# Optimization experiments

Measured on AMD Instinct MI355X. Metric: run time of the kernel, lower is better.

## Reference

```python
import jax, jax.numpy as jnp
import numpy as np

DIM = 1024
HEADS = 16
HEAD_DIM = DIM // HEADS
NUM_FILTERS = 4
NUM_TAPS = 101
RES = 512

def setup_inputs() -> dict:
    key = jax.random.key(0)
    ks = jax.random.split(key, 5)
    B, S = 2, 2048
    x = jax.random.normal(ks[0], (B, S, DIM), dtype=jnp.float32)
    Wqkv = jax.random.normal(ks[1], (3 * DIM, DIM), dtype=jnp.float32) * (DIM ** -0.5)
    Wout = jax.random.normal(ks[2], (DIM, DIM), dtype=jnp.float32) * (DIM ** -0.5)
    Wpos = jax.random.normal(ks[3], (HEADS, NUM_FILTERS), dtype=jnp.float32) * 0.5
    coeffs = jax.random.normal(ks[4], (NUM_FILTERS, NUM_TAPS), dtype=jnp.float32) * 0.05
    return {"x": x, "Wqkv": Wqkv, "Wout": Wout, "Wpos": Wpos, "coeffs": coeffs}

def _fir_fft(c, sig):
    # c: (T,), sig: (R,) -> causal FFT convolution, first R samples
    R = sig.shape[0]
    L = R + c.shape[0] - 1
    out = jnp.fft.ifft(jnp.fft.fft(sig, n=L) * jnp.fft.fft(c, n=L)).real
    return out[:R]

def reference(x, Wqkv, Wout, Wpos, coeffs):
    B, S, D = x.shape
    scale = HEAD_DIM ** -0.5

    # filtered prototype table: (R, F)
    proto = jnp.linspace(0.0, 1.0, RES).astype(x.dtype)
    table = jax.vmap(_fir_fft, in_axes=(0, None))(coeffs, proto).T  # (R, F)

    # relative-distance index matrix (S, S), constants derived from static shape
    r = jnp.arange(S)
    rel = jnp.abs(r[None, :] - r[:, None]).astype(jnp.float32) / max(S - 1, 1)
    idx = jnp.clip(jnp.round(rel * (RES - 1)).astype(jnp.int32), 0, RES - 1)

    pos_feat = table[idx]                                   # (S, S, F)
    pos_bias = jnp.einsum('ijf,hf->hij', pos_feat, Wpos)    # (H, S, S)

    qkv = jnp.einsum('bsd,ed->bse', x, Wqkv)                # (B, S, 3D)
    q, k, v = jnp.split(qkv, 3, axis=-1)
    q = q.reshape(B, S, HEADS, HEAD_DIM)
    k = k.reshape(B, S, HEADS, HEAD_DIM)
    v = v.reshape(B, S, HEADS, HEAD_DIM)

    logits = jnp.einsum('bihd,bjhd->bhij', q, k) * scale + pos_bias[None]
    attn = jax.nn.softmax(logits, axis=-1)
    out = jnp.einsum('bhij,bjhd->bihd', attn, v).reshape(B, S, D)
    return jnp.einsum('bsd,ed->bse', out, Wout)
```

## Files before the change

kernel.cpp:

```cpp
#include <hip/hip_runtime.h>
#include <hip/hip_bf16.h>
#include <cstddef>

#define SEQ     2048
#define BATCH   2
#define DIMSZ   1024
#define HEADS   16
#define HDIM    64
#define E3      3072
#define RESN    512
#define NTAPS   101
#define NFILT   4
#define MROWS   (BATCH * SEQ)
#define LOG2E   1.44269504088896340736f

typedef __attribute__((ext_vector_type(8))) short bf16x8;
typedef __attribute__((ext_vector_type(4))) float f32x4;

__device__ __forceinline__ unsigned short f2bf(float f) {
  unsigned u = __float_as_uint(f);
  u += 0x7fffu + ((u >> 16) & 1u);
  return (unsigned short)(u >> 16);
}
__device__ __forceinline__ float bf2f(unsigned short h) {
  return __uint_as_float(((unsigned)h) << 16);
}
__device__ __forceinline__ void split2(float f, unsigned short& h, unsigned short& l) {
  h = f2bf(f);
  l = f2bf(f - bf2f(h));
}
__device__ __forceinline__ unsigned pkbf(float a, float b) {
  __hip_bfloat162 t = __float22bfloat162_rn(float2{a, b});
  union { __hip_bfloat162 h; unsigned u; } cv; cv.h = t;
  return cv.u;
}
__device__ __forceinline__ void async16(void* lds, const void* g) {
  __builtin_amdgcn_global_load_lds(
      (const __attribute__((address_space(1))) unsigned int*)g,
      (__attribute__((address_space(3))) unsigned int*)lds, 16, 0, 0);
}

__global__ __launch_bounds__(256) void cvt_bf16_kern(
    const float* __restrict__ src, unsigned short* __restrict__ dst, int n)
{
  const int i = (blockIdx.x * 256 + threadIdx.x) * 8;
  if (i >= n) return;
  const float4 a = *(const float4*)(src + i);
  const float4 b = *(const float4*)(src + i + 4);
  ushort4 p = {f2bf(a.x), f2bf(a.y), f2bf(a.z), f2bf(a.w)};
  ushort4 q = {f2bf(b.x), f2bf(b.y), f2bf(b.z), f2bf(b.w)};
  *(ushort4*)(dst + i)     = p;
  *(ushort4*)(dst + i + 4) = q;
}

__global__ __launch_bounds__(256) void split_pair_kern(
    const float* __restrict__ src, unsigned short* __restrict__ hi,
    unsigned short* __restrict__ lo, int n)
{
  const int i = (blockIdx.x * 256 + threadIdx.x) * 4;
  if (i >= n) return;
  const float4 a = *(const float4*)(src + i);
  ushort4 h, l;
  split2(a.x, h.x, l.x); split2(a.y, h.y, l.y);
  split2(a.z, h.z, l.z); split2(a.w, h.w, l.w);
  *(ushort4*)(hi + i) = h;
  *(ushort4*)(lo + i) = l;
}

__global__ __launch_bounds__(256) void pbias_kernel(
    const float* __restrict__ coeffs, const float* __restrict__ Wpos,
    float* __restrict__ pbias2)
{
  __shared__ float table[RESN][NFILT];
  const int h = blockIdx.x;
  const int tid = threadIdx.x;
  for (int rf = tid; rf < RESN * NFILT; rf += 256) {
    const int r = rf >> 2, f = rf & 3;
    const int tmax = r < (NTAPS - 1) ? r : (NTAPS - 1);
    float s = 0.f;
    for (int t = 0; t <= tmax; ++t)
      s += coeffs[f * NTAPS + t] * ((float)(r - t) * (1.0f / (float)(RESN - 1)));
    table[r][f] = s;
  }
  __syncthreads();
  float wp[NFILT];
#pragma unroll
  for (int f = 0; f < NFILT; ++f) wp[f] = Wpos[h * NFILT + f];
  for (int d = tid; d < SEQ; d += 256) {
    const float rel = (float)d / (float)(SEQ - 1);
    int idx = (int)rintf(rel * (float)(RESN - 1));
    idx = idx < 0 ? 0 : (idx > RESN - 1 ? RESN - 1 : idx);
    float s = 0.f;
#pragma unroll
    for (int f = 0; f < NFILT; ++f) s += table[idx][f] * wp[f];
    pbias2[h * SEQ + d] = s * LOG2E;
  }
}

__global__ __launch_bounds__(256) void gemm_bf16(
    const unsigned short* __restrict__ A, const unsigned short* __restrict__ B,
    unsigned short* __restrict__ C, int M, int N, int K)
{
  __shared__ unsigned short As[128][32];
  __shared__ unsigned short Bs[128][32];
  const int tid = threadIdx.x;
  const int lane = tid & 63;
  const int w = tid >> 6, wm = w >> 1, wn = w & 1;
  const int c = lane & 15, G = lane >> 4;
  const int m0 = blockIdx.y * 128, n0 = blockIdx.x * 128;

  const int srow = lane >> 2;
  const int scol = (lane & 3) << 3;

  f32x4 acc[4][4];
#pragma unroll
  for (int mf = 0; mf < 4; ++mf)
#pragma unroll
    for (int nf = 0; nf < 4; ++nf) acc[mf][nf] = (f32x4){0.f, 0.f, 0.f, 0.f};

  for (int k0 = 0; k0 < K; k0 += 32) {
    __syncthreads();
#pragma unroll
    for (int r = 0; r < 2; ++r) {
      const int chunk = r * 4 + w;
      const int row = (chunk << 4) + srow;
      async16(&As[chunk << 4][0], A + (size_t)(m0 + row) * K + k0 + scol);
      async16(&Bs[chunk << 4][0], B + (size_t)(n0 + row) * K + k0 + scol);
    }
    __syncthreads();

    bf16x8 fa[4], fb[4];
#pragma unroll
    for (int mf = 0; mf < 4; ++mf)
      fa[mf] = *(const bf16x8*)&As[wm * 64 + 16 * mf + c][8 * G];
#pragma unroll
    for (int nf = 0; nf < 4; ++nf)
      fb[nf] = *(const bf16x8*)&Bs[wn * 64 + 16 * nf + c][8 * G];
#pragma unroll
    for (int nf = 0; nf < 4; ++nf)
#pragma unroll
      for (int mf = 0; mf < 4; ++mf)
        acc[mf][nf] = __builtin_amdgcn_mfma_f32_16x16x32_bf16(fa[mf], fb[nf], acc[mf][nf], 0, 0, 0);
  }

#pragma unroll
  for (int mf = 0; mf < 4; ++mf)
#pragma unroll
    for (int nf = 0; nf < 4; ++nf)
#pragma unroll
      for (int r = 0; r < 4; ++r)
        C[(size_t)(m0 + wm * 64 + 16 * mf + 4 * G + r) * N + n0 + wn * 64 + 16 * nf + c] =
            f2bf(acc[mf][nf][r]);
}

__global__ __launch_bounds__(256) void gemm_split3(
    const unsigned short* __restrict__ Ah, const unsigned short* __restrict__ Al,
    const unsigned short* __restrict__ Bh, const unsigned short* __restrict__ Bl,
    float* __restrict__ C, int M, int N, int K)
{
  __shared__ unsigned short AhS[128][32], AlS[128][32];
  __shared__ unsigned short BhS[128][32], BlS[128][32];
  const int tid = threadIdx.x;
  const int lane = tid & 63;
  const int w = tid >> 6, wm = w >> 1, wn = w & 1;
  const int c = lane & 15, G = lane >> 4;
  const int m0 = blockIdx.y * 128, n0 = blockIdx.x * 128;

  const int srow = lane >> 2;
  const int scol = (lane & 3) << 3;

  f32x4 acc[4][4];
#pragma unroll
  for (int mf = 0; mf < 4; ++mf)
#pragma unroll
    for (int nf = 0; nf < 4; ++nf) acc[mf][nf] = (f32x4){0.f, 0.f, 0.f, 0.f};

  for (int k0 = 0; k0 < K; k0 += 32) {
    __syncthreads();
#pragma unroll
    for (int r = 0; r < 2; ++r) {
      const int chunk = r * 4 + w;
      const int row = (chunk << 4) + srow;
      const size_t oa = (size_t)(m0 + row) * K + k0 + scol;
      const size_t ob = (size_t)(n0 + row) * K + k0 + scol;
      async16(&AhS[chunk << 4][0], Ah + oa);
      async16(&AlS[chunk << 4][0], Al + oa);
      async16(&BhS[chunk << 4][0], Bh + ob);
      async16(&BlS[chunk << 4][0], Bl + ob);
    }
    __syncthreads();

    bf16x8 fah[4], fal[4];
#pragma unroll
    for (int mf = 0; mf < 4; ++mf) {
      fah[mf] = *(const bf16x8*)&AhS[wm * 64 + 16 * mf + c][8 * G];
      fal[mf] = *(const bf16x8*)&AlS[wm * 64 + 16 * mf + c][8 * G];
    }
#pragma unroll
    for (int nf = 0; nf < 4; ++nf) {
      const bf16x8 fbh = *(const bf16x8*)&BhS[wn * 64 + 16 * nf + c][8 * G];
      const bf16x8 fbl = *(const bf16x8*)&BlS[wn * 64 + 16 * nf + c][8 * G];
#pragma unroll
      for (int mf = 0; mf < 4; ++mf) {
        acc[mf][nf] = __builtin_amdgcn_mfma_f32_16x16x32_bf16(fah[mf], fbh, acc[mf][nf], 0, 0, 0);
        acc[mf][nf] = __builtin_amdgcn_mfma_f32_16x16x32_bf16(fah[mf], fbl, acc[mf][nf], 0, 0, 0);
        acc[mf][nf] = __builtin_amdgcn_mfma_f32_16x16x32_bf16(fal[mf], fbh, acc[mf][nf], 0, 0, 0);
      }
    }
  }

#pragma unroll
  for (int mf = 0; mf < 4; ++mf)
#pragma unroll
    for (int nf = 0; nf < 4; ++nf)
#pragma unroll
      for (int r = 0; r < 4; ++r)
        C[(size_t)(m0 + wm * 64 + 16 * mf + 4 * G + r) * N + n0 + wn * 64 + 16 * nf + c] =
            acc[mf][nf][r];
}

__global__ __launch_bounds__(256) void attn_pure(
    const unsigned short* __restrict__ qkv,
    const float* __restrict__ pbias2,
    unsigned short* __restrict__ ao_hi,
    unsigned short* __restrict__ ao_lo)
{
  __shared__ unsigned short Kh[64][64];
  __shared__ unsigned short Vh[64][64];
  __shared__ unsigned short Ps[64][64];
  __shared__ float pb[SEQ];

  const int tid = threadIdx.x;
  const int lane = tid & 63;
  const int w = tid >> 6;
  const int c = lane & 15, G = lane >> 4;
  const int bh = blockIdx.y, b = bh >> 4, h = bh & 15;
  const int i0 = blockIdx.x * 64;
  const int i_glob = i0 + w * 16 + c;
  const float scale2 = 0.125f * LOG2E;

  for (int idx = tid * 4; idx < SEQ; idx += 1024)
    *(float4*)&pb[idx] = *(const float4*)(pbias2 + h * SEQ + idx);

  bf16x8 qb[2];
#pragma unroll
  for (int ks = 0; ks < 2; ++ks)
    qb[ks] = *(const bf16x8*)(qkv + (size_t)(b * SEQ + i_glob) * E3 + h * HDIM + 32 * ks + 8 * G);

  f32x4 oacc[4];
#pragma unroll
  for (int nf = 0; nf < 4; ++nf) oacc[nf] = (f32x4){0.f, 0.f, 0.f, 0.f};
  float mi = -1e30f, li = 0.f;

  const int vd8 = 8 * (tid & 7);
  const int vjp = 2 * (tid >> 3);

  const int klrow = lane >> 3;
  const int klsl  = lane & 7;

  for (int jt = 0; jt < SEQ / 64; ++jt) {
    const int j0 = jt * 64;
    const size_t rowK = (size_t)(b * SEQ + j0) * E3 + DIMSZ + h * HDIM;
    const size_t rowV = (size_t)(b * SEQ + j0) * E3 + 2 * DIMSZ + h * HDIM;

    const bf16x8 v0 = *(const bf16x8*)(qkv + rowV + (size_t)vjp * E3 + vd8);
    const bf16x8 v1 = *(const bf16x8*)(qkv + rowV + (size_t)(vjp + 1) * E3 + vd8);

    __syncthreads();

#pragma unroll
    for (int r = 0; r < 2; ++r) {
      const int chunk = r * 4 + w;
      const int krow = (chunk << 3) + klrow;
      const int ksl = klsl ^ (krow & 7);
      async16(&Kh[chunk << 3][0], qkv + rowK + (size_t)krow * E3 + 8 * ksl);
    }
#pragma unroll
    for (int e = 0; e < 8; ++e) {
      const int d = vd8 + e;
      const unsigned pk = (unsigned)(unsigned short)v0[e] |
                          ((unsigned)(unsigned short)v1[e] << 16);
      const int col = (((vjp >> 3) ^ (d & 7)) << 3) | (vjp & 7);
      *(unsigned*)&Vh[d][col] = pk;
    }
    __syncthreads();

    f32x4 st[4];
#pragma unroll
    for (int mf = 0; mf < 4; ++mf) st[mf] = (f32x4){0.f, 0.f, 0.f, 0.f};
#pragma unroll
    for (int ks = 0; ks < 2; ++ks)
#pragma unroll
      for (int mf = 0; mf < 4; ++mf) {
        const int sr = (4 * ks + G) ^ (c & 7);
        const bf16x8 ka = *(const bf16x8*)&Kh[16 * mf + c][8 * sr];
        st[mf] = __builtin_amdgcn_mfma_f32_16x16x32_bf16(ka, qb[ks], st[mf], 0, 0, 0);
      }

    float p[16];
    float rm = -1e30f;
#pragma unroll
    for (int mf = 0; mf < 4; ++mf)
#pragma unroll
      for (int r = 0; r < 4; ++r) {
        const int j = j0 + 16 * mf + 4 * G + r;
        const int d = i_glob > j ? i_glob - j : j - i_glob;
        const float lg = fmaf(st[mf][r], scale2, pb[d]);
        p[mf * 4 + r] = lg;
        rm = fmaxf(rm, lg);
      }
    rm = fmaxf(rm, __shfl_xor(rm, 16));
    rm = fmaxf(rm, __shfl_xor(rm, 32));
    const float newm = fmaxf(mi, rm);
    const float fr = exp2f(mi - newm);
    float rs = 0.f;
#pragma unroll
    for (int t = 0; t < 16; ++t) {
      p[t] = exp2f(p[t] - newm);
      rs += p[t];
    }
    rs += __shfl_xor(rs, 16);
    rs += __shfl_xor(rs, 32);
    li = li * fr + rs;
    mi = newm;
    float frr[4];
#pragma unroll
    for (int r = 0; r < 4; ++r) frr[r] = __shfl(fr, 20 * G + r);
#pragma unroll
    for (int nf = 0; nf < 4; ++nf)
#pragma unroll
      for (int r = 0; r < 4; ++r) oacc[nf][r] *= frr[r];

#pragma unroll
    for (int mf = 0; mf < 4; ++mf) {
      const int sw = (2 * mf + (G >> 1)) ^ (c & 7);
      uint2 pw = {pkbf(p[4 * mf + 0], p[4 * mf + 1]),
                  pkbf(p[4 * mf + 2], p[4 * mf + 3])};
      *(uint2*)&Ps[16 * w + c][8 * sw + 4 * (G & 1)] = pw;
    }

#pragma unroll
    for (int ks = 0; ks < 2; ++ks) {
      const int spr = (4 * ks + G) ^ (c & 7);
      const bf16x8 pa = *(const bf16x8*)&Ps[16 * w + c][8 * spr];
#pragma unroll
      for (int nf = 0; nf < 4; ++nf) {
        const int d = 16 * nf + c;
        const int sv = (4 * ks + G) ^ (d & 7);
        const bf16x8 vb = *(const bf16x8*)&Vh[d][8 * sv];
        oacc[nf] = __builtin_amdgcn_mfma_f32_16x16x32_bf16(pa, vb, oacc[nf], 0, 0, 0);
      }
    }
  }

  float rinv[4];
#pragma unroll
  for (int r = 0; r < 4; ++r) rinv[r] = 1.0f / __shfl(li, 20 * G + r);
#pragma unroll
  for (int nf = 0; nf < 4; ++nf)
#pragma unroll
    for (int r = 0; r < 4; ++r) {
      const float v = oacc[nf][r] * rinv[r];
      const size_t off = (size_t)(b * SEQ + i0 + 16 * w + 4 * G + r) * DIMSZ +
                         h * HDIM + 16 * nf + c;
      unsigned short vh, vl;
      split2(v, vh, vl);
      ao_hi[off] = vh;
      ao_lo[off] = vl;
    }
}

extern "C" void kernel_launch(void* const* d_in, const int* in_sizes, int n_in,
                              void* d_out, int out_size, void* d_ws, size_t ws_size,
                              hipStream_t stream) {
  const float* x      = (const float*)d_in[0];
  const float* Wqkv   = (const float*)d_in[1];
  const float* Wout   = (const float*)d_in[2];
  const float* Wpos   = (const float*)d_in[3];
  const float* coeffs = (const float*)d_in[4];
  float* out = (float*)d_out;

  unsigned short* qkv_bf  = (unsigned short*)d_ws;
  unsigned short* x_bf    = qkv_bf + (size_t)MROWS * E3;
  unsigned short* wqkv_bf = x_bf + (size_t)MROWS * DIMSZ;
  unsigned short* wout_h  = wqkv_bf + (size_t)E3 * DIMSZ;
  unsigned short* wout_l  = wout_h + (size_t)DIMSZ * DIMSZ;
  unsigned short* ao_h    = wout_l + (size_t)DIMSZ * DIMSZ;
  unsigned short* ao_l    = ao_h + (size_t)MROWS * DIMSZ;
  float* pbias2 = (float*)(ao_l + (size_t)MROWS * DIMSZ);

  const int nx = MROWS * DIMSZ;
  const int nw = E3 * DIMSZ;
  const int no = DIMSZ * DIMSZ;

  cvt_bf16_kern<<<nx / 2048, 256, 0, stream>>>(x, x_bf, nx);
  cvt_bf16_kern<<<nw / 2048, 256, 0, stream>>>(Wqkv, wqkv_bf, nw);
  split_pair_kern<<<no / 1024, 256, 0, stream>>>(Wout, wout_h, wout_l, no);
  pbias_kernel<<<HEADS, 256, 0, stream>>>(coeffs, Wpos, pbias2);

  dim3 g1(E3 / 128, MROWS / 128);
  gemm_bf16<<<g1, 256, 0, stream>>>(x_bf, wqkv_bf, qkv_bf, MROWS, E3, DIMSZ);

  dim3 g2(SEQ / 64, BATCH * HEADS);
  attn_pure<<<g2, 256, 0, stream>>>(qkv_bf, pbias2, ao_h, ao_l);

  dim3 g3(DIMSZ / 128, MROWS / 128);
  gemm_split3<<<g3, 256, 0, stream>>>(ao_h, ao_l, wout_h, wout_l, out, MROWS, DIMSZ, DIMSZ);
}
```

Baseline: 337.4 us.

## Double-buffer GEMM tiles, swizzle block order, shrink output GEMM tiles, use fast exp2

Both GEMMs now double-buffer their LDS tiles so the next K-slice loads asynchronously while MFMAs run on the current one, and they remap block indices with an XCD-style swizzle. The split3 output GEMM moves from 128x128 to 64x64 tiles, which quadruples the block count to fill the GPU better at the cost of more operand reloads. Launch bounds gain an occupancy hint of 4, and attention uses the raw hardware exp2 builtin in place of exp2f. The risks are register pressure from the occupancy hints and a different cache locality pattern from the swizzle.

```diff
diff --git a/kernel.cpp b/kernel.cpp
--- a/kernel.cpp
+++ b/kernel.cpp
@@ -39,6 +39,7 @@
       (const __attribute__((address_space(1))) unsigned int*)g,
       (__attribute__((address_space(3))) unsigned int*)lds, 16, 0, 0);
 }
+#define EXP2(x) __builtin_amdgcn_exp2f(x)
 
 __global__ __launch_bounds__(256) void cvt_bf16_kern(
     const float* __restrict__ src, unsigned short* __restrict__ dst, int n)
@@ -97,20 +98,27 @@
   }
 }
 
-__global__ __launch_bounds__(256) void gemm_bf16(
+__global__ __launch_bounds__(256, 4) void gemm_bf16(
     const unsigned short* __restrict__ A, const unsigned short* __restrict__ B,
     unsigned short* __restrict__ C, int M, int N, int K)
 {
-  __shared__ unsigned short As[128][32];
-  __shared__ unsigned short Bs[128][32];
+  __shared__ unsigned short As[2][128][32];
+  __shared__ unsigned short Bs[2][128][32];
   const int tid = threadIdx.x;
   const int lane = tid & 63;
   const int w = tid >> 6, wm = w >> 1, wn = w & 1;
   const int c = lane & 15, G = lane >> 4;
-  const int m0 = blockIdx.y * 128, n0 = blockIdx.x * 128;
+
+  const int nwg = gridDim.x * gridDim.y;
+  const int bid = blockIdx.y * gridDim.x + blockIdx.x;
+  const int swz = (bid & 7) * (nwg >> 3) + (bid >> 3);
+  const int bx = swz % gridDim.x, by = swz / gridDim.x;
+  const int m0 = by * 128, n0 = bx * 128;
 
   const int srow = lane >> 2;
   const int scol = (lane & 3) << 3;
+  const unsigned short* Ab = A + (size_t)m0 * K;
+  const unsigned short* Bb = B + (size_t)n0 * K;
 
   f32x4 acc[4][4];
 #pragma unroll
@@ -118,29 +126,36 @@
 #pragma unroll
     for (int nf = 0; nf < 4; ++nf) acc[mf][nf] = (f32x4){0.f, 0.f, 0.f, 0.f};
 
-  for (int k0 = 0; k0 < K; k0 += 32) {
-    __syncthreads();
+  auto stage = [&](int buf, int k0) {
 #pragma unroll
     for (int r = 0; r < 2; ++r) {
       const int chunk = r * 4 + w;
       const int row = (chunk << 4) + srow;
-      async16(&As[chunk << 4][0], A + (size_t)(m0 + row) * K + k0 + scol);
-      async16(&Bs[chunk << 4][0], B + (size_t)(n0 + row) * K + k0 + scol);
-    }
-    __syncthreads();
-
+      async16(&As[buf][chunk << 4][0], Ab + (size_t)row * K + k0 + scol);
+      async16(&Bs[buf][chunk << 4][0], Bb + (size_t)row * K + k0 + scol);
+    }
+  };
+
+  stage(0, 0);
+  __syncthreads();
+  int cur = 0;
+  const int NT = K >> 5;
+  for (int t = 0; t < NT; ++t) {
+    if (t + 1 < NT) stage(cur ^ 1, (t + 1) << 5);
     bf16x8 fa[4], fb[4];
 #pragma unroll
     for (int mf = 0; mf < 4; ++mf)
-      fa[mf] = *(const bf16x8*)&As[wm * 64 + 16 * mf + c][8 * G];
+      fa[mf] = *(const bf16x8*)&As[cur][wm * 64 + 16 * mf + c][8 * G];
 #pragma unroll
     for (int nf = 0; nf < 4; ++nf)
-      fb[nf] = *(const bf16x8*)&Bs[wn * 64 + 16 * nf + c][8 * G];
+      fb[nf] = *(const bf16x8*)&Bs[cur][wn * 64 + 16 * nf + c][8 * G];
 #pragma unroll
     for (int nf = 0; nf < 4; ++nf)
 #pragma unroll
       for (int mf = 0; mf < 4; ++mf)
         acc[mf][nf] = __builtin_amdgcn_mfma_f32_16x16x32_bf16(fa[mf], fb[nf], acc[mf][nf], 0, 0, 0);
+    __syncthreads();
+    cur ^= 1;
   }
 
 #pragma unroll
@@ -153,73 +168,82 @@
             f2bf(acc[mf][nf][r]);
 }
 
-__global__ __launch_bounds__(256) void gemm_split3(
+__global__ __launch_bounds__(256, 4) void gemm_split3(
     const unsigned short* __restrict__ Ah, const unsigned short* __restrict__ Al,
     const unsigned short* __restrict__ Bh, const unsigned short* __restrict__ Bl,
     float* __restrict__ C, int M, int N, int K)
 {
-  __shared__ unsigned short AhS[128][32], AlS[128][32];
-  __shared__ unsigned short BhS[128][32], BlS[128][32];
+  __shared__ unsigned short AhS[2][64][32], AlS[2][64][32];
+  __shared__ unsigned short BhS[2][64][32], BlS[2][64][32];
   const int tid = threadIdx.x;
   const int lane = tid & 63;
   const int w = tid >> 6, wm = w >> 1, wn = w & 1;
   const int c = lane & 15, G = lane >> 4;
-  const int m0 = blockIdx.y * 128, n0 = blockIdx.x * 128;
+
+  const int nwg = gridDim.x * gridDim.y;
+  const int bid = blockIdx.y * gridDim.x + blockIdx.x;
+  const int swz = (bid & 7) * (nwg >> 3) + (bid >> 3);
+  const int bx = swz % gridDim.x, by = swz / gridDim.x;
+  const int m0 = by * 64, n0 = bx * 64;
 
   const int srow = lane >> 2;
   const int scol = (lane & 3) << 3;
 
-  f32x4 acc[4][4];
-#pragma unroll
-  for (int mf = 0; mf < 4; ++mf)
-#pragma unroll
-    for (int nf = 0; nf < 4; ++nf) acc[mf][nf] = (f32x4){0.f, 0.f, 0.f, 0.f};
-
-  for (int k0 = 0; k0 < K; k0 += 32) {
+  f32x4 acc[2][2];
+#pragma unroll
+  for (int mf = 0; mf < 2; ++mf)
+#pragma unroll
+    for (int nf = 0; nf < 2; ++nf) acc[mf][nf] = (f32x4){0.f, 0.f, 0.f, 0.f};
+
+  auto stage = [&](int buf, int k0) {
+    const int arow = m0 + 16 * w + srow;
+    const int brow = n0 + 16 * w + srow;
+    async16(&AhS[buf][16 * w][0], Ah + (size_t)arow * K + k0 + scol);
+    async16(&AlS[buf][16 * w][0], Al + (size_t)arow * K + k0 + scol);
+    async16(&BhS[buf][16 * w][0], Bh + (size_t)brow * K + k0 + scol);
+    async16(&BlS[buf][16 * w][0], Bl + (size_t)brow * K + k0 + scol);
+  };
+
+  stage(0, 0);
+  __syncthreads();
+  int cur = 0;
+  const int NT = K >> 5;
+  for (int t = 0; t < NT; ++t) {
+    if (t + 1 < NT) stage(cur ^ 1, (t + 1) << 5);
+    bf16x8 fah[2], fal[2], fbh[2], fbl[2];
+#pragma unroll
+    for (int mf = 0; mf < 2; ++mf) {
+      fah[mf] = *(const bf16x8*)&AhS[cur][32 * wm + 16 * mf + c][8 * G];
+      fal[mf] = *(const bf16x8*)&AlS[cur][32 * wm + 16 * mf + c][8 * G];
+    }
+#pragma unroll
+    for (int nf = 0; nf < 2; ++nf) {
+      fbh[nf] = *(const bf16x8*)&BhS[cur][32 * wn + 16 * nf + c][8 * G];
+      fbl[nf] = *(const bf16x8*)&BlS[cur][32 * wn + 16 * nf + c][8 * G];
+    }
+#pragma unroll
+    for (int nf = 0; nf < 2; ++nf)
+#pragma unroll
+      for (int mf = 0; mf < 2; ++mf) {
+        acc[mf][nf] = __builtin_amdgcn_mfma_f32_16x16x32_bf16(fah[mf], fbh[nf], acc[mf][nf], 0, 0, 0);
+        acc[mf][nf] = __builtin_amdgcn_mfma_f32_16x16x32_bf16(fah[mf], fbl[nf], acc[mf][nf], 0, 0, 0);
+        acc[mf][nf] = __builtin_amdgcn_mfma_f32_16x16x32_bf16(fal[mf], fbh[nf], acc[mf][nf], 0, 0, 0);
+      }
     __syncthreads();
-#pragma unroll
-    for (int r = 0; r < 2; ++r) {
-      const int chunk = r * 4 + w;
-      const int row = (chunk << 4) + srow;
-      const size_t oa = (size_t)(m0 + row) * K + k0 + scol;
-      const size_t ob = (size_t)(n0 + row) * K + k0 + scol;
-      async16(&AhS[chunk << 4][0], Ah + oa);
-      async16(&AlS[chunk << 4][0], Al + oa);
-      async16(&BhS[chunk << 4][0], Bh + ob);
-      async16(&BlS[chunk << 4][0], Bl + ob);
-    }
-    __syncthreads();
-
-    bf16x8 fah[4], fal[4];
-#pragma unroll
-    for (int mf = 0; mf < 4; ++mf) {
-      fah[mf] = *(const bf16x8*)&AhS[wm * 64 + 16 * mf + c][8 * G];
-      fal[mf] = *(const bf16x8*)&AlS[wm * 64 + 16 * mf + c][8 * G];
-    }
-#pragma unroll
-    for (int nf = 0; nf < 4; ++nf) {
-      const bf16x8 fbh = *(const bf16x8*)&BhS[wn * 64 + 16 * nf + c][8 * G];
-      const bf16x8 fbl = *(const bf16x8*)&BlS[wn * 64 + 16 * nf + c][8 * G];
-#pragma unroll
-      for (int mf = 0; mf < 4; ++mf) {
-        acc[mf][nf] = __builtin_amdgcn_mfma_f32_16x16x32_bf16(fah[mf], fbh, acc[mf][nf], 0, 0, 0);
-        acc[mf][nf] = __builtin_amdgcn_mfma_f32_16x16x32_bf16(fah[mf], fbl, acc[mf][nf], 0, 0, 0);
-        acc[mf][nf] = __builtin_amdgcn_mfma_f32_16x16x32_bf16(fal[mf], fbh, acc[mf][nf], 0, 0, 0);
-      }
-    }
+    cur ^= 1;
   }
 
 #pragma unroll
-  for (int mf = 0; mf < 4; ++mf)
-#pragma unroll
-    for (int nf = 0; nf < 4; ++nf)
+  for (int mf = 0; mf < 2; ++mf)
+#pragma unroll
+    for (int nf = 0; nf < 2; ++nf)
 #pragma unroll
       for (int r = 0; r < 4; ++r)
-        C[(size_t)(m0 + wm * 64 + 16 * mf + 4 * G + r) * N + n0 + wn * 64 + 16 * nf + c] =
+        C[(size_t)(m0 + 32 * wm + 16 * mf + 4 * G + r) * N + n0 + 32 * wn + 16 * nf + c] =
             acc[mf][nf][r];
 }
 
-__global__ __launch_bounds__(256) void attn_pure(
+__global__ __launch_bounds__(256, 4) void attn_pure(
     const unsigned short* __restrict__ qkv,
     const float* __restrict__ pbias2,
     unsigned short* __restrict__ ao_hi,
@@ -254,7 +278,6 @@
 
   const int vd8 = 8 * (tid & 7);
   const int vjp = 2 * (tid >> 3);
-
   const int klrow = lane >> 3;
   const int klsl  = lane & 7;
 
@@ -312,11 +335,11 @@
     rm = fmaxf(rm, __shfl_xor(rm, 16));
     rm = fmaxf(rm, __shfl_xor(rm, 32));
     const float newm = fmaxf(mi, rm);
-    const float fr = exp2f(mi - newm);
+    const float fr = EXP2(mi - newm);
     float rs = 0.f;
 #pragma unroll
     for (int t = 0; t < 16; ++t) {
-      p[t] = exp2f(p[t] - newm);
+      p[t] = EXP2(p[t] - newm);
       rs += p[t];
     }
     rs += __shfl_xor(rs, 16);
@@ -404,6 +427,6 @@
   dim3 g2(SEQ / 64, BATCH * HEADS);
   attn_pure<<<g2, 256, 0, stream>>>(qkv_bf, pbias2, ao_h, ao_l);
 
-  dim3 g3(DIMSZ / 128, MROWS / 128);
+  dim3 g3(DIMSZ / 64, MROWS / 64);
   gemm_split3<<<g3, 256, 0, stream>>>(ao_h, ao_l, wout_h, wout_l, out, MROWS, DIMSZ, DIMSZ);
 }
```

Result: faster. 318.1 us (-5.7%).
